# Kernel optimization log

Hardware: AMD Instinct MI355X
Metric: run time of the kernel (lower is better)

Reference implementation:

```python
import jax, jax.numpy as jnp
import numpy as np

N = 4096
DIM = 128      # dim_in
HID = 256      # mlp hidden_dim
K_IN = 8       # k for linear_k

def _knn_edges(dist, k):
    # dist: [n,n]; k nearest neighbors excluding self (matches heapq loop)
    n = dist.shape[0]
    d = jnp.where(jnp.eye(n, dtype=bool), jnp.inf, dist)
    nbr = jax.lax.top_k(-d, k)[1]                     # [n,k] indices of k smallest
    src = jnp.repeat(jnp.arange(n), k)                # res[0] = i
    dst = nbr.reshape(-1)                             # res[1] = neighbor
    return src, dst

def _gcn_conv(x, src, dst, W, b):
    # torch_geometric GCNConv: add self loops + symmetric normalization
    n = x.shape[0]
    loop = jnp.arange(n)
    s = jnp.concatenate([src, loop])
    t = jnp.concatenate([dst, loop])
    xw = x @ W
    deg = jax.ops.segment_sum(jnp.ones(s.shape[0], x.dtype), t, num_segments=n)
    dinv = jax.lax.rsqrt(deg)                         # deg >= 1 due to self loops
    norm = dinv[s] * dinv[t]
    out = jax.ops.segment_sum(norm[:, None] * xw[s], t, num_segments=n)
    return out + b

def _gcn(x, src, dst, Wg1, bg1, Wg2, bg2):
    h = jax.nn.relu(_gcn_conv(x, src, dst, Wg1, bg1))
    h = _gcn_conv(h, src, dst, Wg2, bg2)              # dropout is identity in eval
    return jax.nn.log_softmax(h, axis=1)

def _conv2d(x, w, b):
    y = jax.lax.conv_general_dilated(x, w, (1, 1), 'SAME',
        dimension_numbers=('NCHW', 'OIHW', 'NCHW'))
    return y + b.reshape(1, -1, 1, 1)

def setup_inputs():
    key = jax.random.key(0)
    ks = jax.random.split(key, 20)
    f32 = jnp.float32
    def w(k, shape):
        fan = shape[0]
        return (jax.random.uniform(k, shape, f32) * 2 - 1) * (1.0 / np.sqrt(fan))
    return {
        'data_x_1': jax.random.normal(ks[0], (1, N, 4), f32),
        'data_x_2': jax.random.normal(ks[1], (1, N, K_IN, 4), f32),
        'Wk': w(ks[2], (K_IN, 1)),        'bk': jnp.zeros((1,), f32),
        'Wg1': w(ks[3], (8, DIM // 2)),   'bg1': jnp.zeros((DIM // 2,), f32),
        'Wg2': w(ks[4], (DIM // 2, DIM)), 'bg2': jnp.zeros((DIM,), f32),
        'Wq': w(ks[5], (3 * DIM, DIM)),   'bq': jnp.zeros((DIM,), f32),
        'Wkey': w(ks[6], (3 * DIM, DIM)), 'bkey': jnp.zeros((DIM,), f32),
        'Woff': w(ks[7], (4, DIM)),       'boff': jnp.zeros((DIM,), f32),
        'pw': jnp.full((1,), 0.25, f32),
        'Wf1': w(ks[8], (DIM, HID)),      'bf1': jnp.zeros((HID,), f32),
        'Wf2': w(ks[9], (HID, HID)),      'bf2': jnp.zeros((HID,), f32),
        'Wf3': w(ks[10], (HID, 4)),       'bf3': jnp.zeros((4,), f32),
        'Wcy3': w(ks[11], (1, 1, 1, 3)),  'bcy3': jnp.zeros((1,), f32),
        'Wcx3': w(ks[12], (1, 1, 3, 1)),  'bcx3': jnp.zeros((1,), f32),
        'Wcy5': w(ks[13], (1, 1, 1, 5)),  'bcy5': jnp.zeros((1,), f32),
        'Wcx5': w(ks[14], (1, 1, 5, 1)),  'bcx5': jnp.zeros((1,), f32),
        'Wcy9': w(ks[15], (1, 1, 1, 9)),  'bcy9': jnp.zeros((1,), f32),
        'Wcx9': w(ks[16], (1, 1, 9, 1)),  'bcx9': jnp.zeros((1,), f32),
    }

def reference(data_x_1, data_x_2, Wk, bk, Wg1, bg1, Wg2, bg2, Wq, bq, Wkey, bkey,
              Woff, boff, pw, Wf1, bf1, Wf2, bf2, Wf3, bf3,
              Wcy3, bcy3, Wcx3, bcx3, Wcy5, bcy5, Wcx5, bcx5, Wcy9, bcy9, Wcx9, bcx9):
    # linear_k over k dimension: [1,n,k,4] -> transpose -> [1,n,4,k] -> [1,n,4]
    dx2 = jnp.swapaxes(data_x_2, 2, 3)
    dx2_out = (dx2 @ Wk + bk)[..., 0]
    data_x = jnp.concatenate([data_x_1, dx2_out], axis=2)   # [1,n,8]
    Ot = data_x[:, :, 4:]                                   # [1,n,4]

    pos = data_x[:, :, 0:2]
    diff = pos[:, :, None, :] - pos[:, None, :, :]          # [1,n,n,2]
    distances = jnp.linalg.norm(diff, axis=3)               # [1,n,n]
    maxd = jnp.max(distances, axis=2, keepdims=True)
    oushi_atte = 1.0 - distances / maxd                     # [1,n,n]

    x0 = data_x[0]
    dist0 = jax.lax.stop_gradient(distances[0])             # knn on detached dist
    embs = []
    for kk in (3, 5, 9):
        src, dst = _knn_edges(dist0, kk)
        embs.append(_gcn(x0, src, dst, Wg1, bg1, Wg2, bg2)[None])
    embedding = jnp.concatenate(embs, axis=2)               # [1,n,3*DIM]

    query = embedding @ Wq + bq                             # [1,n,DIM]
    key_t = embedding @ Wkey + bkey
    scores = jnp.einsum('bnd,bmd->bnm', query, key_t) / jnp.sqrt(jnp.float32(DIM))
    A = scores / jnp.max(scores, axis=2, keepdims=True)     # [1,n,n]

    A4 = A[None]                                            # [1,1,n,n]
    c3 = _conv2d(A4, Wcy3, bcy3) + _conv2d(A4, Wcx3, bcx3)
    c5 = _conv2d(A4, Wcy5, bcy5) + _conv2d(A4, Wcx5, bcx5)
    c9 = _conv2d(A4, Wcy9, bcy9) + _conv2d(A4, Wcx9, bcx9)

    A_cat = jnp.concatenate([A, oushi_atte, c3[0], c5[0], c9[0]], axis=2)  # [1,n,5n]
    A_cat = (A_cat - A_cat.min()) / (A_cat.max() - A_cat.min())

    Ot5 = jnp.tile(Ot, (1, 5, 1))                           # [1,5n,4]
    h = jnp.matmul(A_cat, Ot5)                              # [1,n,4]
    h = h @ Woff + boff                                     # [1,n,DIM]
    h = jnp.where(h > 0, h, pw * h)                         # PReLU (scalar weight)
    h = jax.nn.relu(h @ Wf1 + bf1)
    h = jax.nn.relu(h @ Wf2 + bf2)
    return h @ Wf3 + bf3                                    # [1,n,4]
```

## Files before the change

### kernel.cpp

```cpp
#include <hip/hip_runtime.h>
#include <math.h>

#define NN 4096

typedef __bf16 bf16x8 __attribute__((ext_vector_type(8)));
typedef float  f32x4  __attribute__((ext_vector_type(4)));

static __device__ __forceinline__ unsigned enc_f(float f){
    unsigned u = __float_as_uint(f);
    return (u & 0x80000000u) ? ~u : (u | 0x80000000u);
}
static __device__ __forceinline__ float dec_f(unsigned u){
    unsigned b = (u & 0x80000000u) ? (u & 0x7fffffffu) : ~u;
    return __uint_as_float(b);
}
static __device__ __forceinline__ float4 shfl4(float4 v, int src){
    float4 r;
    r.x = __shfl(v.x, src, 64);
    r.y = __shfl(v.y, src, 64);
    r.z = __shfl(v.z, src, 64);
    r.w = __shfl(v.w, src, 64);
    return r;
}
static __device__ __forceinline__ unsigned long long shflx_u64(unsigned long long v, int m){
    unsigned lo = __shfl_xor((unsigned)(v & 0xffffffffu), m, 64);
    unsigned hi = __shfl_xor((unsigned)(v >> 32), m, 64);
    return ((unsigned long long)hi << 32) | lo;
}

__global__ void k_prep(const float* __restrict__ dx1, const float* __restrict__ dx2,
                       const float* __restrict__ Wk, const float* __restrict__ bk,
                       float* __restrict__ x0, float* __restrict__ colsum,
                       float2* __restrict__ pos, float4* __restrict__ otp){
    int n = blockIdx.x*blockDim.x + threadIdx.x;
    if (n >= NN) return;
    float wk[8];
    #pragma unroll
    for (int j=0;j<8;j++) wk[j] = Wk[j];
    float bkv = bk[0];
    float4 d1 = *(const float4*)&dx1[n*4];
    pos[n] = make_float2(d1.x, d1.y);
    #pragma unroll
    for (int c=0;c<4;c++) x0[n*8+c] = (&d1.x)[c];
    float4 ot;
    #pragma unroll
    for (int c=0;c<4;c++){
        float acc = bkv;
        #pragma unroll
        for (int j=0;j<8;j++) acc += dx2[(n*8+j)*4+c]*wk[j];
        x0[n*8+4+c] = acc;
        (&ot.x)[c] = acc;
        atomicAdd(&colsum[c], acc);
    }
    otp[n] = ot;
}

__global__ void k_ty(const float* __restrict__ x0,
        const float* __restrict__ Wcy3, const float* __restrict__ Wcy5, const float* __restrict__ Wcy9,
        float* __restrict__ Ty){
    int j = blockIdx.x*256 + threadIdx.x;
    if (j >= NN) return;
    float Cy[9];
    #pragma unroll
    for (int o=-4;o<=4;o++){
        float c = Wcy9[o+4];
        if (o>=-2 && o<=2) c += Wcy5[o+2];
        if (o>=-1 && o<=1) c += Wcy3[o+1];
        Cy[o+4] = c;
    }
    float4 acc = {0,0,0,0};
    #pragma unroll
    for (int o=-4;o<=4;o++){
        int jj = j - o;
        if ((unsigned)jj < NN){
            float4 ot = *(const float4*)&x0[jj*8+4];
            float c = Cy[o+4];
            acc.x += c*ot.x; acc.y += c*ot.y; acc.z += c*ot.z; acc.w += c*ot.w;
        }
    }
    *(float4*)&Ty[j*4] = acc;
}

#define KCAP 192
__global__ __launch_bounds__(256) void k_dist(const float2* __restrict__ pos,
        const float4* __restrict__ otp,
        float* __restrict__ maxd, int* __restrict__ nbr,
        int* __restrict__ cnt3, int* __restrict__ cnt5, int* __restrict__ cnt9,
        float* __restrict__ dOt){
    __shared__ unsigned long long cbuf[4][KCAP];
    int tid = threadIdx.x;
    int w = tid >> 6, lane = tid & 63;
    int i = blockIdx.x*4 + w;
    float2 pi = pos[i];

    float lmax = 0.f, lmin = INFINITY;
    float4 dacc = {0,0,0,0};
    for (int t=0;t<64;t++){
        int j = (t<<6) | lane;
        float2 p = pos[j];
        float dx = pi.x - p.x, dy = pi.y - p.y;
        float d = sqrtf(dx*dx + dy*dy);
        lmax = fmaxf(lmax, d);
        float4 otj = otp[j];
        dacc.x += d*otj.x; dacc.y += d*otj.y; dacc.z += d*otj.z; dacc.w += d*otj.w;
        if (j != i) lmin = fminf(lmin, d);
    }
    #pragma unroll
    for (int m=1;m<64;m<<=1){
        lmax = fmaxf(lmax, __shfl_xor(lmax, m, 64));
        dacc.x += __shfl_xor(dacc.x, m, 64);
        dacc.y += __shfl_xor(dacc.y, m, 64);
        dacc.z += __shfl_xor(dacc.z, m, 64);
        dacc.w += __shfl_xor(dacc.w, m, 64);
    }
    if (lane==0){
        maxd[i] = lmax;
        *(float4*)&dOt[i*4] = dacc;
    }
    float v = lmin, T = 0.f;
    #pragma unroll
    for (int r=0;r<9;r++){
        float m = v;
        #pragma unroll
        for (int s=1;s<64;s<<=1) m = fminf(m, __shfl_xor(m, s, 64));
        T = m;
        if (v == m) v = INFINITY;
    }

    int base = 0;
    for (int t=0;t<64;t++){
        int j = (t<<6) | lane;
        float2 p = pos[j];
        float dx = pi.x - p.x, dy = pi.y - p.y;
        float d = sqrtf(dx*dx + dy*dy);
        bool pass = (j != i) && (d <= T);
        unsigned long long b = __ballot(pass);
        if (b){
            int pre = __popcll(b & ((1ull<<lane)-1ull));
            int idx = base + pre;
            if (pass && idx < KCAP)
                cbuf[w][idx] = ((unsigned long long)__float_as_uint(d) << 32) | (unsigned)j;
            base += __popcll(b);
        }
    }
    int M = base < KCAP ? base : KCAP;

    unsigned long long c0 = (lane      < M) ? cbuf[w][lane]      : ~0ULL;
    unsigned long long c1 = (lane+64   < M) ? cbuf[w][lane+64]   : ~0ULL;
    unsigned long long c2 = (lane+128  < M) ? cbuf[w][lane+128]  : ~0ULL;
    for (int r=0;r<9;r++){
        unsigned long long mv = c0 < c1 ? c0 : c1;
        mv = mv < c2 ? mv : c2;
        #pragma unroll
        for (int s=1;s<64;s<<=1){
            unsigned long long o = shflx_u64(mv, s);
            if (o < mv) mv = o;
        }
        if (c0 == mv) c0 = ~0ULL;
        else if (c1 == mv) c1 = ~0ULL;
        else if (c2 == mv) c2 = ~0ULL;
        if (lane == 0){
            int j = (int)(mv & 0xffffffffu);
            nbr[i*9+r] = j;
            atomicAdd(&cnt9[j], 1);
            if (r<5) atomicAdd(&cnt5[j], 1);
            if (r<3) atomicAdd(&cnt3[j], 1);
        }
    }
}

__global__ __launch_bounds__(256) void k_scan(const int* __restrict__ cnt3,
        const int* __restrict__ cnt5, const int* __restrict__ cnt9,
        int* __restrict__ offc, float* __restrict__ dinvc){
    __shared__ int part[256];
    int tid = threadIdx.x;
    for (int g=0; g<3; g++){
        const int* cp = g==0?cnt3:(g==1?cnt5:cnt9);
        int base = tid*16;
        int loc[16]; int s=0;
        #pragma unroll
        for (int q=0;q<16;q++){ loc[q]=s; s += cp[base+q]; }
        part[tid]=s; __syncthreads();
        for (int d=1; d<256; d<<=1){
            int v = (tid>=d) ? part[tid-d] : 0;
            __syncthreads();
            part[tid] += v;
            __syncthreads();
        }
        int pre = (tid==0) ? 0 : part[tid-1];
        #pragma unroll
        for (int q=0;q<16;q++){
            offc[g*NN + base + q]  = pre + loc[q];
            dinvc[g*NN + base + q] = rsqrtf((float)cp[base+q] + 1.f);
        }
        __syncthreads();
    }
}

__global__ void k_fill(const int* __restrict__ nbr, const int* __restrict__ offc,
        int* __restrict__ cur, int* __restrict__ rev){
    int i = blockIdx.x*256 + threadIdx.x;
    if (i >= NN) return;
    #pragma unroll
    for (int t=0;t<9;t++){
        int j = nbr[i*9+t];
        int gmin = t<3 ? 0 : (t<5 ? 1 : 2);
        for (int g=gmin; g<3; g++){
            int pos = atomicAdd(&cur[g*NN+j], 1);
            int rb = (g==0) ? 0 : (g==1 ? NN*3 : NN*8);
            rev[rb + offc[g*NN+j] + pos] = i;
        }
    }
}

__global__ void k_y1(const float* __restrict__ x0, const float* __restrict__ Wg1,
                     float* __restrict__ xw){
    int idx = blockIdx.x*256 + threadIdx.x;
    if (idx >= NN*64) return;
    int n = idx>>6, c = idx&63;
    float acc = 0.f;
    #pragma unroll
    for (int k=0;k<8;k++) acc += x0[n*8+k]*Wg1[k*64+c];
    xw[idx] = acc;
}

__global__ __launch_bounds__(256) void k_h1y2(const float* __restrict__ xw,
        const int* __restrict__ offc,
        const int* __restrict__ cnt3, const int* __restrict__ cnt5, const int* __restrict__ cnt9,
        const int* __restrict__ rev, const float* __restrict__ dinvc,
        const float* __restrict__ bg1, const float* __restrict__ Wg2,
        float* __restrict__ y2){
    __shared__ float h1s[12][64];
    int n0 = blockIdx.x*4, tid = threadIdx.x;
    for (int s=tid; s<768; s+=256){
        int p = s>>6, k = s&63, g = p>>2, n = n0+(p&3);
        const int* cp = g==0?cnt3:(g==1?cnt5:cnt9);
        int rb = (g==0) ? 0 : (g==1 ? NN*3 : NN*8);
        int cnt = cp[n];
        int o = rb + offc[g*NN+n];
        float dv = dinvc[g*NN+n];
        float srow = dv*xw[n*64+k];
        for (int e=0;e<cnt;e++){
            int i = rev[o+e];
            srow += dinvc[g*NN+i]*xw[i*64+k];
        }
        float v = dv*srow + bg1[k];
        h1s[p][k] = v>0.f ? v : 0.f;
    }
    __syncthreads();
    int c = tid & 127, ph = tid>>7;
    float a6[6] = {0,0,0,0,0,0};
    for (int k=0;k<64;k++){
        float w = Wg2[k*128+c];
        #pragma unroll
        for (int q=0;q<6;q++) a6[q] += h1s[q*2+ph][k]*w;
    }
    #pragma unroll
    for (int q=0;q<6;q++){
        int p = q*2+ph, g = p>>2, n = n0+(p&3);
        float dv = dinvc[g*NN+n];
        y2[(size_t)g*NN*128 + (size_t)n*128 + c] = dv*a6[q];
    }
}

__global__ __launch_bounds__(128) void k_fin(const float* __restrict__ y2,
        const int* __restrict__ offc,
        const int* __restrict__ cnt3, const int* __restrict__ cnt5, const int* __restrict__ cnt9,
        const int* __restrict__ rev, const float* __restrict__ dinvc,
        const float* __restrict__ bg2, float* __restrict__ emb){
    __shared__ float sm[2], ss[2];
    int b = blockIdx.x;
    int n = b & (NN-1), g = b >> 12;
    const int* cp = g==0?cnt3:(g==1?cnt5:cnt9);
    int rb = (g==0) ? 0 : (g==1 ? NN*3 : NN*8);
    int cnt = cp[n];
    int o = rb + offc[g*NN+n];
    float dv = dinvc[g*NN+n];
    int c = threadIdx.x;
    const float* yg = y2 + (size_t)g*NN*128;
    float s = yg[(size_t)n*128 + c];
    for (int e=0;e<cnt;e++){
        int i = rev[o+e];
        s += yg[(size_t)i*128 + c];
    }
    float v = dv*s + bg2[c];
    float m = v;
    #pragma unroll
    for (int st=1;st<64;st<<=1) m = fmaxf(m, __shfl_xor(m, st, 64));
    if ((c&63)==0) sm[c>>6] = m;
    __syncthreads();
    m = fmaxf(sm[0], sm[1]);
    float e = expf(v - m);
    float t = e;
    #pragma unroll
    for (int st=1;st<64;st<<=1) t += __shfl_xor(t, st, 64);
    if ((c&63)==0) ss[c>>6] = t;
    __syncthreads();
    t = ss[0]+ss[1];
    emb[n*384 + g*128 + c] = v - m - logf(t);
}

__global__ __launch_bounds__(256) void k_qk(const float* __restrict__ emb,
        const float* __restrict__ Wq, const float* __restrict__ bq,
        const float* __restrict__ Wkey, const float* __restrict__ bkey,
        __bf16* __restrict__ qh, __bf16* __restrict__ ql,
        __bf16* __restrict__ kh, __bf16* __restrict__ kl){
    __shared__ float es[8][384];
    int n0 = blockIdx.x*8;
    int tid = threadIdx.x;
    for (int idx=tid; idx<8*384; idx+=256){
        int m = idx/384, k = idx%384;
        es[m][k] = emb[(n0+m)*384+k];
    }
    __syncthreads();
    int c = tid & 127;
    int sel = tid >> 7;
    const float* W = sel ? Wkey : Wq;
    float b = sel ? bkey[c] : bq[c];
    float acc[8];
    #pragma unroll
    for (int m=0;m<8;m++) acc[m]=b;
    for (int k=0;k<384;k++){
        float w = W[k*128+c];
        #pragma unroll
        for (int m=0;m<8;m++) acc[m] += es[m][k]*w;
    }
    __bf16* oh = sel ? kh : qh;
    __bf16* ol = sel ? kl : ql;
    #pragma unroll
    for (int m=0;m<8;m++){
        float v = acc[m];
        __bf16 h = (__bf16)v;
        oh[(size_t)(n0+m)*128+c] = h;
        ol[(size_t)(n0+m)*128+c] = (__bf16)(v - (float)h);
    }
}

__global__ __launch_bounds__(256) void k_scores(
        const __bf16* __restrict__ qh, const __bf16* __restrict__ ql,
        const __bf16* __restrict__ kh, const __bf16* __restrict__ kl,
        float* __restrict__ scores,
        unsigned* __restrict__ rowmaxenc, unsigned* __restrict__ rowminenc){
    int bx = blockIdx.x & 31;
    int by = blockIdx.x >> 5;
    int tid = threadIdx.x;
    int w = tid >> 6, lane = tid & 63;
    int li = lane & 15, g = lane >> 4;
    int r0 = by*128 + (w>>1)*64;
    int c0 = bx*128 + (w&1)*64;

    f32x4 acc[4][4] = {};
    for (int ks=0; ks<4; ++ks){
        int kofs = ks*32 + g*8;
        bf16x8 ah[4], al[4], bh[4], bl[4];
        #pragma unroll
        for (int f=0; f<4; ++f){
            ah[f] = *(const bf16x8*)&qh[(size_t)(r0+f*16+li)*128 + kofs];
            al[f] = *(const bf16x8*)&ql[(size_t)(r0+f*16+li)*128 + kofs];
            bh[f] = *(const bf16x8*)&kh[(size_t)(c0+f*16+li)*128 + kofs];
            bl[f] = *(const bf16x8*)&kl[(size_t)(c0+f*16+li)*128 + kofs];
        }
        #pragma unroll
        for (int fr=0; fr<4; ++fr){
            #pragma unroll
            for (int fc=0; fc<4; ++fc){
                acc[fr][fc] = __builtin_amdgcn_mfma_f32_16x16x32_bf16(ah[fr], bh[fc], acc[fr][fc], 0, 0, 0);
                acc[fr][fc] = __builtin_amdgcn_mfma_f32_16x16x32_bf16(ah[fr], bl[fc], acc[fr][fc], 0, 0, 0);
                acc[fr][fc] = __builtin_amdgcn_mfma_f32_16x16x32_bf16(al[fr], bh[fc], acc[fr][fc], 0, 0, 0);
            }
        }
    }
    #pragma unroll
    for (int fr=0; fr<4; ++fr){
        #pragma unroll
        for (int r=0; r<4; ++r){
            int row = r0 + fr*16 + g*4 + r;
            float mx = -INFINITY, mn = INFINITY;
            #pragma unroll
            for (int fc=0; fc<4; ++fc){
                float v = acc[fr][fc][r];
                scores[(size_t)row*NN + c0 + fc*16 + li] = v;
                mx = fmaxf(mx, v);
                mn = fminf(mn, v);
            }
            #pragma unroll
            for (int s=1; s<16; s<<=1){
                mx = fmaxf(mx, __shfl_xor(mx, s, 64));
                mn = fminf(mn, __shfl_xor(mn, s, 64));
            }
            if (li == 0){
                atomicMax(&rowmaxenc[row], enc_f(mx));
                atomicMin(&rowminenc[row], enc_f(mn));
            }
        }
    }
}

__global__ void k_invr(const unsigned* __restrict__ rowmaxenc, float* __restrict__ invr){
    int i = blockIdx.x*256 + threadIdx.x;
    if (i >= NN) return;
    invr[i] = 1.f/dec_f(rowmaxenc[i]);
}

__global__ __launch_bounds__(256) void k_cconv(const float* __restrict__ scores,
        const float* __restrict__ invr,
        const float* __restrict__ Wcy3, const float* __restrict__ Wcx3,
        const float* __restrict__ Wcy5, const float* __restrict__ Wcx5,
        const float* __restrict__ Wcy9, const float* __restrict__ Wcx9,
        const float* __restrict__ bcy3, const float* __restrict__ bcx3,
        const float* __restrict__ bcy5, const float* __restrict__ bcx5,
        const float* __restrict__ bcy9, const float* __restrict__ bcx9,
        float* __restrict__ mnmx){
    __shared__ float smn[4], smx[4];
    int tid = threadIdx.x;
    int w = tid >> 6, lane = tid & 63;
    int strip = blockIdx.x;
    int i0 = (blockIdx.y*4 + w)*19;
    int colbase = strip*248 - 4 + lane*4;
    bool lv = (colbase >= 0) && (colbase + 3 < NN);
    bool outLane = (lane >= 1) && (lane < 63) && lv;

    float wy3[3],wx3[3],wy5[5],wx5[5],wy9[9],wx9[9];
    #pragma unroll
    for (int t=0;t<3;t++){ wy3[t]=Wcy3[t]; wx3[t]=Wcx3[t]; }
    #pragma unroll
    for (int t=0;t<5;t++){ wy5[t]=Wcy5[t]; wx5[t]=Wcx5[t]; }
    #pragma unroll
    for (int t=0;t<9;t++){ wy9[t]=Wcy9[t]; wx9[t]=Wcx9[t]; }
    float bc3 = bcy3[0]+bcx3[0];
    float bc5 = bcy5[0]+bcx5[0];
    float bc9 = bcy9[0]+bcx9[0];

    float4 win[9];
    float mn = INFINITY, mx = -INFINITY;
    const int laneL = lane - 1, laneR = lane + 1;

    for (int tb = 0; tb < 3; ++tb){
        #pragma unroll
        for (int u = 0; u < 9; ++u){
            int t  = tb*9 + u;
            int ri = i0 - 4 + t;
            float4 a = make_float4(0,0,0,0);
            if (((unsigned)ri < NN) && lv){
                float iv = invr[ri];
                float4 v = *(const float4*)&scores[(size_t)ri*NN + colbase];
                a.x = v.x*iv; a.y = v.y*iv; a.z = v.z*iv; a.w = v.w*iv;
            }
            win[u] = a;
            int ro = i0 + t - 8;
            if (t >= 8 && ro < NN){
                float4 ctr = win[(u+5)%9];
                float4 wl = shfl4(ctr, laneL);
                float4 wr = shfl4(ctr, laneR);
                if (outLane){
                    float cw[12] = {wl.x,wl.y,wl.z,wl.w, ctr.x,ctr.y,ctr.z,ctr.w, wr.x,wr.y,wr.z,wr.w};
                    #pragma unroll
                    for (int c=0;c<4;c++){
                        float cx9 = ((win[(u+1)%9][c]*wx9[0] + win[(u+2)%9][c]*wx9[1]) + (win[(u+3)%9][c]*wx9[2] + win[(u+4)%9][c]*wx9[3]))
                                  + ((win[(u+5)%9][c]*wx9[4] + win[(u+6)%9][c]*wx9[5]) + (win[(u+7)%9][c]*wx9[6] + win[(u+8)%9][c]*wx9[7]))
                                  + win[u][c]*wx9[8];
                        float cx5 = ((win[(u+3)%9][c]*wx5[0] + win[(u+4)%9][c]*wx5[1]) + (win[(u+5)%9][c]*wx5[2] + win[(u+6)%9][c]*wx5[3]))
                                  + win[(u+7)%9][c]*wx5[4];
                        float cx3 = (win[(u+4)%9][c]*wx3[0] + win[(u+5)%9][c]*wx3[1]) + win[(u+6)%9][c]*wx3[2];
                        float cy9 = ((cw[c+0]*wy9[0] + cw[c+1]*wy9[1]) + (cw[c+2]*wy9[2] + cw[c+3]*wy9[3]))
                                  + ((cw[c+4]*wy9[4] + cw[c+5]*wy9[5]) + (cw[c+6]*wy9[6] + cw[c+7]*wy9[7]))
                                  + cw[c+8]*wy9[8];
                        float cy5 = ((cw[c+2]*wy5[0] + cw[c+3]*wy5[1]) + (cw[c+4]*wy5[2] + cw[c+5]*wy5[3]))
                                  + cw[c+6]*wy5[4];
                        float cy3 = (cw[c+3]*wy3[0] + cw[c+4]*wy3[1]) + cw[c+5]*wy3[2];
                        float c3v = cy3+cx3+bc3, c5v = cy5+cx5+bc5, c9v = cy9+cx9+bc9;
                        mn = fminf(mn, fminf(fminf(c3v,c5v),c9v));
                        mx = fmaxf(mx, fmaxf(fmaxf(c3v,c5v),c9v));
                    }
                }
            }
        }
    }
    #pragma unroll
    for (int m=1; m<64; m<<=1){
        mn = fminf(mn, __shfl_xor(mn, m, 64));
        mx = fmaxf(mx, __shfl_xor(mx, m, 64));
    }
    if (lane == 0){ smn[w] = mn; smx[w] = mx; }
    __syncthreads();
    if (tid == 0){
        float a0 = fminf(fminf(smn[0],smn[1]), fminf(smn[2],smn[3]));
        float b0 = fmaxf(fmaxf(smx[0],smx[1]), fmaxf(smx[2],smx[3]));
        int bid = blockIdx.y*gridDim.x + blockIdx.x;
        mnmx[bid] = a0;
        mnmx[1024 + bid] = b0;
    }
}

__global__ __launch_bounds__(256) void k_kot(const __bf16* __restrict__ kh, const __bf16* __restrict__ kl,
        const float* __restrict__ x0, const float* __restrict__ Ty,
        float* __restrict__ kOt){
    __shared__ float red[256][8];
    int d = blockIdx.x, tid = threadIdx.x;
    float a[8] = {0,0,0,0,0,0,0,0};
    for (int j = tid; j < NN; j += 256){
        float kv = (float)kh[(size_t)j*128 + d] + (float)kl[(size_t)j*128 + d];
        float4 ot = *(const float4*)&x0[j*8+4];
        float4 ty = *(const float4*)&Ty[j*4];
        a[0] += kv*ot.x; a[1] += kv*ot.y; a[2] += kv*ot.z; a[3] += kv*ot.w;
        a[4] += kv*ty.x; a[5] += kv*ty.y; a[6] += kv*ty.z; a[7] += kv*ty.w;
    }
    #pragma unroll
    for (int q=0;q<8;q++) red[tid][q] = a[q];
    __syncthreads();
    for (int s=128; s>0; s>>=1){
        if (tid < s){
            #pragma unroll
            for (int q=0;q<8;q++) red[tid][q] += red[tid+s][q];
        }
        __syncthreads();
    }
    if (tid < 8) kOt[d*8 + tid] = red[0][tid];
}

__global__ __launch_bounds__(256) void k_asd(
        const __bf16* __restrict__ qh, const __bf16* __restrict__ ql,
        const float* __restrict__ kOt,
        const unsigned* __restrict__ rowmaxenc, const float* __restrict__ maxd,
        const float* __restrict__ dOt, const float* __restrict__ colsum,
        const float* __restrict__ bcy3, const float* __restrict__ bcx3,
        const float* __restrict__ bcy5, const float* __restrict__ bcx5,
        const float* __restrict__ bcy9, const float* __restrict__ bcx9,
        float* __restrict__ ASdot, float* __restrict__ Bv){
    __shared__ float kst[128*8];
    int tid = threadIdx.x;
    for (int s = tid; s < 1024; s += 256) kst[s] = kOt[s];
    __syncthreads();
    int lane = tid & 63, r = tid >> 6;
    int i = blockIdx.x*4 + r;
    float a[8] = {0,0,0,0,0,0,0,0};
    #pragma unroll
    for (int dd=0; dd<2; ++dd){
        int d = lane + dd*64;
        float qv = (float)qh[(size_t)i*128 + d] + (float)ql[(size_t)i*128 + d];
        #pragma unroll
        for (int q=0;q<8;q++) a[q] += qv * kst[d*8+q];
    }
    #pragma unroll
    for (int m=1; m<64; m<<=1){
        #pragma unroll
        for (int q=0;q<8;q++) a[q] += __shfl_xor(a[q], m, 64);
    }
    if (lane == 0){
        float iv = 1.f/dec_f(rowmaxenc[i]);
        float imv = 1.f/maxd[i];
        float bcsum = bcy3[0]+bcx3[0]+bcy5[0]+bcx5[0]+bcy9[0]+bcx9[0];
        float k = 1.f + bcsum;
        float4 cs = *(const float4*)colsum;
        float4 dv = *(const float4*)&dOt[i*4];
        float4 pa = {iv*a[0], iv*a[1], iv*a[2], iv*a[3]};
        float4 b;
        b.x = cs.x*k - imv*dv.x + iv*a[4];
        b.y = cs.y*k - imv*dv.y + iv*a[5];
        b.z = cs.z*k - imv*dv.z + iv*a[6];
        b.w = cs.w*k - imv*dv.w + iv*a[7];
        *(float4*)&ASdot[i*4] = pa;
        *(float4*)&Bv[i*4]    = b;
    }
}

__global__ __launch_bounds__(256) void k_gmm(const float* __restrict__ mnmx,
        const unsigned* __restrict__ rowminenc, const unsigned* __restrict__ rowmaxenc,
        float* __restrict__ gmm){
    __shared__ float smn[256], smx[256];
    int tid = threadIdx.x;
    float mn = 0.f, mx = 1.f;
    for (int i=tid; i<NN; i+=256){
        float rmx = dec_f(rowmaxenc[i]);
        float q = dec_f(rowminenc[i]) / rmx;
        mn = fminf(mn, fminf(1.f, q));
        mx = fmaxf(mx, fmaxf(1.f, q));
    }
    for (int b=tid; b<918; b+=256){
        mn = fminf(mn, mnmx[b]);
        mx = fmaxf(mx, mnmx[1024+b]);
    }
    smn[tid]=mn; smx[tid]=mx; __syncthreads();
    for (int s=128;s>0;s>>=1){
        if (tid<s){ smn[tid]=fminf(smn[tid],smn[tid+s]); smx[tid]=fmaxf(smx[tid],smx[tid+s]); }
        __syncthreads();
    }
    if (tid==0){ gmm[0]=smn[0]; gmm[1]=smx[0]; }
}

__global__ void k_hfin(const float* __restrict__ ASdot, const float* __restrict__ Bv,
        const float* __restrict__ Wcx3, const float* __restrict__ Wcx5, const float* __restrict__ Wcx9,
        const float* __restrict__ gmm, const float* __restrict__ colsum,
        float* __restrict__ hfin){
    int i = blockIdx.x*256 + threadIdx.x;
    if (i >= NN) return;
    float Cx[9];
    #pragma unroll
    for (int o=-4;o<=4;o++){
        float c = Wcx9[o+4];
        if (o>=-2 && o<=2) c += Wcx5[o+2];
        if (o>=-1 && o<=1) c += Wcx3[o+1];
        Cx[o+4] = c;
    }
    float4 h = *(const float4*)&Bv[i*4];
    float4 a0 = *(const float4*)&ASdot[i*4];
    h.x += a0.x; h.y += a0.y; h.z += a0.z; h.w += a0.w;
    #pragma unroll
    for (int o=-4;o<=4;o++){
        int r = i + o;
        if ((unsigned)r < NN){
            float4 av = *(const float4*)&ASdot[r*4];
            float c = Cx[o+4];
            h.x += c*av.x; h.y += c*av.y; h.z += c*av.z; h.w += c*av.w;
        }
    }
    float mnv = gmm[0], mxv = gmm[1];
    float s = 1.f/(mxv-mnv), oa = -mnv*s;
    float4 cs = *(const float4*)colsum;
    float4 out;
    out.x = s*h.x + 5.f*oa*cs.x;
    out.y = s*h.y + 5.f*oa*cs.y;
    out.z = s*h.z + 5.f*oa*cs.z;
    out.w = s*h.w + 5.f*oa*cs.w;
    *(float4*)&hfin[i*4] = out;
}

__global__ __launch_bounds__(256) void k_mlp(const float* __restrict__ hfin,
        const float* __restrict__ Woff, const float* __restrict__ boff, const float* __restrict__ pw,
        const float* __restrict__ Wf1, const float* __restrict__ bf1,
        const float* __restrict__ Wf2, const float* __restrict__ bf2,
        const float* __restrict__ Wf3, const float* __restrict__ bf3,
        float* __restrict__ out){
    __shared__ float h1[8][128];
    __shared__ float h2[8][256];
    __shared__ float h3[8][256];
    int n0 = blockIdx.x*8, tid = threadIdx.x;
    float p = pw[0];
    {
        int c = tid & 127, mb = (tid>>7)*4;
        #pragma unroll
        for (int mm=0; mm<4; mm++){
            int m = mb+mm;
            float v = boff[c];
            #pragma unroll
            for (int k=0;k<4;k++) v += hfin[(n0+m)*4+k]*Woff[k*128+c];
            h1[m][c] = v>0.f ? v : p*v;
        }
    }
    __syncthreads();
    {
        int c = tid;
        float acc[8];
        #pragma unroll
        for (int m=0;m<8;m++) acc[m] = bf1[c];
        for (int k=0;k<128;k++){
            float w = Wf1[k*256+c];
            #pragma unroll
            for (int m=0;m<8;m++) acc[m] += h1[m][k]*w;
        }
        #pragma unroll
        for (int m=0;m<8;m++) h2[m][c] = acc[m]>0.f?acc[m]:0.f;
    }
    __syncthreads();
    {
        int c = tid;
        float acc[8];
        #pragma unroll
        for (int m=0;m<8;m++) acc[m] = bf2[c];
        for (int k=0;k<256;k++){
            float w = Wf2[k*256+c];
            #pragma unroll
            for (int m=0;m<8;m++) acc[m] += h2[m][k]*w;
        }
        #pragma unroll
        for (int m=0;m<8;m++) h3[m][c] = acc[m]>0.f?acc[m]:0.f;
    }
    __syncthreads();
    int w = tid >> 6, lane = tid & 63;
    #pragma unroll
    for (int mm=0; mm<2; ++mm){
        int m = w*2 + mm;
        float4 acc = {0,0,0,0};
        #pragma unroll
        for (int q=0;q<4;q++){
            int k = lane + q*64;
            float hv = h3[m][k];
            float4 w3 = *(const float4*)&Wf3[k*4];
            acc.x += hv*w3.x; acc.y += hv*w3.y; acc.z += hv*w3.z; acc.w += hv*w3.w;
        }
        #pragma unroll
        for (int s=1; s<64; s<<=1){
            acc.x += __shfl_xor(acc.x, s, 64);
            acc.y += __shfl_xor(acc.y, s, 64);
            acc.z += __shfl_xor(acc.z, s, 64);
            acc.w += __shfl_xor(acc.w, s, 64);
        }
        if (lane == 0){
            float4 o;
            o.x = acc.x + bf3[0]; o.y = acc.y + bf3[1];
            o.z = acc.z + bf3[2]; o.w = acc.w + bf3[3];
            *(float4*)&out[(n0+m)*4] = o;
        }
    }
}

extern "C" void kernel_launch(void* const* d_in, const int* in_sizes, int n_in,
                              void* d_out, int out_size, void* d_ws, size_t ws_size,
                              hipStream_t stream){
    const float* dx1  = (const float*)d_in[0];
    const float* dx2  = (const float*)d_in[1];
    const float* Wk   = (const float*)d_in[2];
    const float* bk   = (const float*)d_in[3];
    const float* Wg1  = (const float*)d_in[4];
    const float* bg1  = (const float*)d_in[5];
    const float* Wg2  = (const float*)d_in[6];
    const float* bg2  = (const float*)d_in[7];
    const float* Wq   = (const float*)d_in[8];
    const float* bq   = (const float*)d_in[9];
    const float* Wkey = (const float*)d_in[10];
    const float* bkey = (const float*)d_in[11];
    const float* Woff = (const float*)d_in[12];
    const float* boff = (const float*)d_in[13];
    const float* pw   = (const float*)d_in[14];
    const float* Wf1  = (const float*)d_in[15];
    const float* bf1  = (const float*)d_in[16];
    const float* Wf2  = (const float*)d_in[17];
    const float* bf2  = (const float*)d_in[18];
    const float* Wf3  = (const float*)d_in[19];
    const float* bf3  = (const float*)d_in[20];
    const float* Wcy3 = (const float*)d_in[21];
    const float* bcy3 = (const float*)d_in[22];
    const float* Wcx3 = (const float*)d_in[23];
    const float* bcx3 = (const float*)d_in[24];
    const float* Wcy5 = (const float*)d_in[25];
    const float* bcy5 = (const float*)d_in[26];
    const float* Wcx5 = (const float*)d_in[27];
    const float* bcx5 = (const float*)d_in[28];
    const float* Wcy9 = (const float*)d_in[29];
    const float* bcy9 = (const float*)d_in[30];
    const float* Wcx9 = (const float*)d_in[31];
    const float* bcx9 = (const float*)d_in[32];

    char* ws = (char*)d_ws;
    size_t off = 0;
    auto alloc = [&](size_t b)->void*{ void* p = ws + off; off += (b + 255) & ~(size_t)255; return p; };

    char* zbase = ws + off;
    float*    colsum    = (float*)   alloc(4*4);
    int*      cnt3      = (int*)     alloc((size_t)NN*4);
    int*      cnt5      = (int*)     alloc((size_t)NN*4);
    int*      cnt9      = (int*)     alloc((size_t)NN*4);
    int*      cur       = (int*)     alloc((size_t)3*NN*4);
    unsigned* rowmaxenc = (unsigned*)alloc((size_t)NN*4);
    size_t zbytes = (size_t)((ws + off) - zbase);
    unsigned* rowminenc = (unsigned*)alloc((size_t)NN*4);

    float*  x0    = (float*) alloc((size_t)NN*8*4);
    float2* pos   = (float2*)alloc((size_t)NN*8);
    float4* otp   = (float4*)alloc((size_t)NN*16);
    float*  maxd  = (float*) alloc((size_t)NN*4);
    int*    nbr   = (int*)   alloc((size_t)NN*9*4);
    int*    offc  = (int*)   alloc((size_t)3*NN*4);
    float*  dinvc = (float*) alloc((size_t)3*NN*4);
    int*    rev   = (int*)   alloc((size_t)NN*17*4);
    float*  xw    = (float*) alloc((size_t)NN*64*4);
    float*  y2    = (float*) alloc((size_t)3*NN*128*4);
    float*  emb   = (float*) alloc((size_t)NN*384*4);
    __bf16* qh    = (__bf16*)alloc((size_t)NN*128*2);
    __bf16* ql    = (__bf16*)alloc((size_t)NN*128*2);
    __bf16* kh    = (__bf16*)alloc((size_t)NN*128*2);
    __bf16* kl    = (__bf16*)alloc((size_t)NN*128*2);
    float* scores = (float*)alloc((size_t)NN*NN*4);
    float* Tyb    = (float*)alloc((size_t)NN*4*4);
    float* invr   = (float*)alloc((size_t)NN*4);
    float* dOt    = (float*)alloc((size_t)NN*4*4);
    float* kOt    = (float*)alloc((size_t)128*8*4);
    float* ASd    = (float*)alloc((size_t)NN*4*4);
    float* Bv     = (float*)alloc((size_t)NN*4*4);
    float* mnmx   = (float*)alloc((size_t)2*1024*4);
    float* gmm    = (float*)alloc(2*4);
    float* hfin   = (float*)alloc((size_t)NN*4*4);
    (void)ws_size; (void)in_sizes; (void)n_in; (void)out_size;

    hipMemsetAsync(zbase, 0, zbytes, stream);
    hipMemsetAsync(rowminenc, 0xFF, (size_t)NN*4, stream);

    k_prep<<<16,256,0,stream>>>(dx1,dx2,Wk,bk,x0,colsum,pos,otp);
    k_ty  <<<16,256,0,stream>>>(x0,Wcy3,Wcy5,Wcy9,Tyb);
    k_dist<<<NN/4,256,0,stream>>>(pos,otp,maxd,nbr,cnt3,cnt5,cnt9,dOt);
    k_scan<<<1,256,0,stream>>>(cnt3,cnt5,cnt9,offc,dinvc);
    k_fill<<<16,256,0,stream>>>(nbr,offc,cur,rev);

    k_y1  <<<NN*64/256,256,0,stream>>>(x0,Wg1,xw);
    k_h1y2<<<NN/4,256,0,stream>>>(xw,offc,cnt3,cnt5,cnt9,rev,dinvc,bg1,Wg2,y2);
    k_fin <<<NN*3,128,0,stream>>>(y2,offc,cnt3,cnt5,cnt9,rev,dinvc,bg2,emb);

    k_qk<<<NN/8,256,0,stream>>>(emb,Wq,bq,Wkey,bkey,qh,ql,kh,kl);
    k_scores<<<1024,256,0,stream>>>(qh,ql,kh,kl,scores,rowmaxenc,rowminenc);
    k_invr<<<16,256,0,stream>>>(rowmaxenc,invr);
    k_kot<<<128,256,0,stream>>>(kh,kl,x0,Tyb,kOt);

    k_cconv<<<dim3(17,54),256,0,stream>>>(scores,invr,
        Wcy3,Wcx3,Wcy5,Wcx5,Wcy9,Wcx9,
        bcy3,bcx3,bcy5,bcx5,bcy9,bcx9, mnmx);
    k_asd<<<NN/4,256,0,stream>>>(qh,ql,kOt,rowmaxenc,maxd,dOt,colsum,
        bcy3,bcx3,bcy5,bcx5,bcy9,bcx9, ASd, Bv);
    k_gmm<<<1,256,0,stream>>>(mnmx,rowminenc,rowmaxenc,gmm);
    k_hfin<<<16,256,0,stream>>>(ASd,Bv,Wcx3,Wcx5,Wcx9,gmm,colsum,hfin);
    k_mlp<<<NN/8,256,0,stream>>>(hfin,Woff,boff,pw,Wf1,bf1,Wf2,bf2,Wf3,bf3,(float*)d_out);
}
```

Measured before the change: 303.5 us.

## Recompute QK scores inside conv kernel instead of materializing full score matrix

The full 4096x4096 fp32 score matrix is no longer written. The first pass now computes only the row max and min. The conv kernel recomputes each 64x64 halo tile of scores with MFMA, scales it by the inverse row max, stages it in LDS and applies the 3/5/9 separable convolutions there to get the min and max. This removes a 64MB write and a 64MB read in exchange for doing the QK matmul twice, with about 30% extra recompute for the halo, plus LDS-based convolution and a larger partial min/max reduction.

```diff
diff --git a/kernel.cpp b/kernel.cpp
--- a/kernel.cpp
+++ b/kernel.cpp
@@ -13,14 +13,6 @@
 static __device__ __forceinline__ float dec_f(unsigned u){
     unsigned b = (u & 0x80000000u) ? (u & 0x7fffffffu) : ~u;
     return __uint_as_float(b);
-}
-static __device__ __forceinline__ float4 shfl4(float4 v, int src){
-    float4 r;
-    r.x = __shfl(v.x, src, 64);
-    r.y = __shfl(v.y, src, 64);
-    r.z = __shfl(v.z, src, 64);
-    r.w = __shfl(v.w, src, 64);
-    return r;
 }
 static __device__ __forceinline__ unsigned long long shflx_u64(unsigned long long v, int m){
     unsigned lo = __shfl_xor((unsigned)(v & 0xffffffffu), m, 64);
@@ -336,34 +328,36 @@
     }
 }
 
-__global__ __launch_bounds__(256) void k_scores(
+__global__ __launch_bounds__(256) void k_qkmm(
         const __bf16* __restrict__ qh, const __bf16* __restrict__ ql,
         const __bf16* __restrict__ kh, const __bf16* __restrict__ kl,
-        float* __restrict__ scores,
         unsigned* __restrict__ rowmaxenc, unsigned* __restrict__ rowminenc){
-    int bx = blockIdx.x & 31;
-    int by = blockIdx.x >> 5;
+    int bx = blockIdx.x & 63;
+    int by = blockIdx.x >> 6;
     int tid = threadIdx.x;
     int w = tid >> 6, lane = tid & 63;
     int li = lane & 15, g = lane >> 4;
     int r0 = by*128 + (w>>1)*64;
-    int c0 = bx*128 + (w&1)*64;
-
-    f32x4 acc[4][4] = {};
+    int c0 = bx*64  + (w&1)*32;
+
+    f32x4 acc[4][2] = {};
     for (int ks=0; ks<4; ++ks){
         int kofs = ks*32 + g*8;
-        bf16x8 ah[4], al[4], bh[4], bl[4];
+        bf16x8 ah[4], al[4], bh[2], bl[2];
         #pragma unroll
         for (int f=0; f<4; ++f){
             ah[f] = *(const bf16x8*)&qh[(size_t)(r0+f*16+li)*128 + kofs];
             al[f] = *(const bf16x8*)&ql[(size_t)(r0+f*16+li)*128 + kofs];
+        }
+        #pragma unroll
+        for (int f=0; f<2; ++f){
             bh[f] = *(const bf16x8*)&kh[(size_t)(c0+f*16+li)*128 + kofs];
             bl[f] = *(const bf16x8*)&kl[(size_t)(c0+f*16+li)*128 + kofs];
         }
         #pragma unroll
         for (int fr=0; fr<4; ++fr){
             #pragma unroll
-            for (int fc=0; fc<4; ++fc){
+            for (int fc=0; fc<2; ++fc){
                 acc[fr][fc] = __builtin_amdgcn_mfma_f32_16x16x32_bf16(ah[fr], bh[fc], acc[fr][fc], 0, 0, 0);
                 acc[fr][fc] = __builtin_amdgcn_mfma_f32_16x16x32_bf16(ah[fr], bl[fc], acc[fr][fc], 0, 0, 0);
                 acc[fr][fc] = __builtin_amdgcn_mfma_f32_16x16x32_bf16(al[fr], bh[fc], acc[fr][fc], 0, 0, 0);
@@ -375,14 +369,8 @@
         #pragma unroll
         for (int r=0; r<4; ++r){
             int row = r0 + fr*16 + g*4 + r;
-            float mx = -INFINITY, mn = INFINITY;
-            #pragma unroll
-            for (int fc=0; fc<4; ++fc){
-                float v = acc[fr][fc][r];
-                scores[(size_t)row*NN + c0 + fc*16 + li] = v;
-                mx = fmaxf(mx, v);
-                mn = fminf(mn, v);
-            }
+            float mx = fmaxf(acc[fr][0][r], acc[fr][1][r]);
+            float mn = fminf(acc[fr][0][r], acc[fr][1][r]);
             #pragma unroll
             for (int s=1; s<16; s<<=1){
                 mx = fmaxf(mx, __shfl_xor(mx, s, 64));
@@ -402,7 +390,9 @@
     invr[i] = 1.f/dec_f(rowmaxenc[i]);
 }
 
-__global__ __launch_bounds__(256) void k_cconv(const float* __restrict__ scores,
+__global__ __launch_bounds__(256) void k_convf(
+        const __bf16* __restrict__ qh, const __bf16* __restrict__ ql,
+        const __bf16* __restrict__ kh, const __bf16* __restrict__ kl,
         const float* __restrict__ invr,
         const float* __restrict__ Wcy3, const float* __restrict__ Wcx3,
         const float* __restrict__ Wcy5, const float* __restrict__ Wcx5,
@@ -411,14 +401,55 @@
         const float* __restrict__ bcy5, const float* __restrict__ bcx5,
         const float* __restrict__ bcy9, const float* __restrict__ bcx9,
         float* __restrict__ mnmx){
+    __shared__ float As[64][68];
     __shared__ float smn[4], smx[4];
+    int bx = blockIdx.x, by = blockIdx.y;
+    int i0 = by*56 - 4;
+    int j0 = bx*56 - 4;
     int tid = threadIdx.x;
     int w = tid >> 6, lane = tid & 63;
-    int strip = blockIdx.x;
-    int i0 = (blockIdx.y*4 + w)*19;
-    int colbase = strip*248 - 4 + lane*4;
-    bool lv = (colbase >= 0) && (colbase + 3 < NN);
-    bool outLane = (lane >= 1) && (lane < 63) && lv;
+    int li = lane & 15, g = lane >> 4;
+
+    f32x4 acc[4] = {};
+    {
+        int col = j0 + w*16 + li;
+        int colc = col < 0 ? 0 : (col > NN-1 ? NN-1 : col);
+        for (int ks=0; ks<4; ++ks){
+            int kofs = ks*32 + g*8;
+            bf16x8 ah[4], al[4], bh, bl;
+            #pragma unroll
+            for (int f=0; f<4; ++f){
+                int row = i0 + f*16 + li;
+                int rowc = row < 0 ? 0 : (row > NN-1 ? NN-1 : row);
+                ah[f] = *(const bf16x8*)&qh[(size_t)rowc*128 + kofs];
+                al[f] = *(const bf16x8*)&ql[(size_t)rowc*128 + kofs];
+            }
+            bh = *(const bf16x8*)&kh[(size_t)colc*128 + kofs];
+            bl = *(const bf16x8*)&kl[(size_t)colc*128 + kofs];
+            #pragma unroll
+            for (int fr=0; fr<4; ++fr){
+                acc[fr] = __builtin_amdgcn_mfma_f32_16x16x32_bf16(ah[fr], bh, acc[fr], 0, 0, 0);
+                acc[fr] = __builtin_amdgcn_mfma_f32_16x16x32_bf16(ah[fr], bl, acc[fr], 0, 0, 0);
+                acc[fr] = __builtin_amdgcn_mfma_f32_16x16x32_bf16(al[fr], bh, acc[fr], 0, 0, 0);
+            }
+        }
+    }
+    {
+        int gcol = j0 + w*16 + li;
+        bool cok = (unsigned)gcol < NN;
+        #pragma unroll
+        for (int fr=0; fr<4; ++fr){
+            #pragma unroll
+            for (int r=0; r<4; ++r){
+                int lr = fr*16 + g*4 + r;
+                int grow = i0 + lr;
+                float v = 0.f;
+                if (cok && (unsigned)grow < NN) v = acc[fr][r] * invr[grow];
+                As[lr][w*16 + li] = v;
+            }
+        }
+    }
+    __syncthreads();
 
     float wy3[3],wx3[3],wy5[5],wx5[5],wy9[9],wx9[9];
     #pragma unroll
@@ -431,49 +462,30 @@
     float bc5 = bcy5[0]+bcx5[0];
     float bc9 = bcy9[0]+bcx9[0];
 
-    float4 win[9];
     float mn = INFINITY, mx = -INFINITY;
-    const int laneL = lane - 1, laneR = lane + 1;
-
-    for (int tb = 0; tb < 3; ++tb){
-        #pragma unroll
-        for (int u = 0; u < 9; ++u){
-            int t  = tb*9 + u;
-            int ri = i0 - 4 + t;
-            float4 a = make_float4(0,0,0,0);
-            if (((unsigned)ri < NN) && lv){
-                float iv = invr[ri];
-                float4 v = *(const float4*)&scores[(size_t)ri*NN + colbase];
-                a.x = v.x*iv; a.y = v.y*iv; a.z = v.z*iv; a.w = v.w*iv;
+    for (int idx = tid; idx < 56*56; idx += 256){
+        int r = (idx/56) + 4, c = (idx%56) + 4;
+        int grow = i0 + r, gcol = j0 + c;
+        if (grow < NN && gcol < NN){
+            float cx9=0.f, cx5=0.f, cx3=0.f;
+            #pragma unroll
+            for (int u=0;u<9;++u){
+                float rv = As[r-4+u][c];
+                cx9 += rv*wx9[u];
+                if (u>=2 && u<=6) cx5 += rv*wx5[u-2];
+                if (u>=3 && u<=5) cx3 += rv*wx3[u-3];
             }
-            win[u] = a;
-            int ro = i0 + t - 8;
-            if (t >= 8 && ro < NN){
-                float4 ctr = win[(u+5)%9];
-                float4 wl = shfl4(ctr, laneL);
-                float4 wr = shfl4(ctr, laneR);
-                if (outLane){
-                    float cw[12] = {wl.x,wl.y,wl.z,wl.w, ctr.x,ctr.y,ctr.z,ctr.w, wr.x,wr.y,wr.z,wr.w};
-                    #pragma unroll
-                    for (int c=0;c<4;c++){
-                        float cx9 = ((win[(u+1)%9][c]*wx9[0] + win[(u+2)%9][c]*wx9[1]) + (win[(u+3)%9][c]*wx9[2] + win[(u+4)%9][c]*wx9[3]))
-                                  + ((win[(u+5)%9][c]*wx9[4] + win[(u+6)%9][c]*wx9[5]) + (win[(u+7)%9][c]*wx9[6] + win[(u+8)%9][c]*wx9[7]))
-                                  + win[u][c]*wx9[8];
-                        float cx5 = ((win[(u+3)%9][c]*wx5[0] + win[(u+4)%9][c]*wx5[1]) + (win[(u+5)%9][c]*wx5[2] + win[(u+6)%9][c]*wx5[3]))
-                                  + win[(u+7)%9][c]*wx5[4];
-                        float cx3 = (win[(u+4)%9][c]*wx3[0] + win[(u+5)%9][c]*wx3[1]) + win[(u+6)%9][c]*wx3[2];
-                        float cy9 = ((cw[c+0]*wy9[0] + cw[c+1]*wy9[1]) + (cw[c+2]*wy9[2] + cw[c+3]*wy9[3]))
-                                  + ((cw[c+4]*wy9[4] + cw[c+5]*wy9[5]) + (cw[c+6]*wy9[6] + cw[c+7]*wy9[7]))
-                                  + cw[c+8]*wy9[8];
-                        float cy5 = ((cw[c+2]*wy5[0] + cw[c+3]*wy5[1]) + (cw[c+4]*wy5[2] + cw[c+5]*wy5[3]))
-                                  + cw[c+6]*wy5[4];
-                        float cy3 = (cw[c+3]*wy3[0] + cw[c+4]*wy3[1]) + cw[c+5]*wy3[2];
-                        float c3v = cy3+cx3+bc3, c5v = cy5+cx5+bc5, c9v = cy9+cx9+bc9;
-                        mn = fminf(mn, fminf(fminf(c3v,c5v),c9v));
-                        mx = fmaxf(mx, fmaxf(fmaxf(c3v,c5v),c9v));
-                    }
-                }
+            float cy9=0.f, cy5=0.f, cy3=0.f;
+            #pragma unroll
+            for (int u=0;u<9;++u){
+                float cv = As[r][c-4+u];
+                cy9 += cv*wy9[u];
+                if (u>=2 && u<=6) cy5 += cv*wy5[u-2];
+                if (u>=3 && u<=5) cy3 += cv*wy3[u-3];
             }
+            float c3v = cy3+cx3+bc3, c5v = cy5+cx5+bc5, c9v = cy9+cx9+bc9;
+            mn = fminf(mn, fminf(fminf(c3v,c5v),c9v));
+            mx = fmaxf(mx, fmaxf(fmaxf(c3v,c5v),c9v));
         }
     }
     #pragma unroll
@@ -486,9 +498,9 @@
     if (tid == 0){
         float a0 = fminf(fminf(smn[0],smn[1]), fminf(smn[2],smn[3]));
         float b0 = fmaxf(fmaxf(smx[0],smx[1]), fmaxf(smx[2],smx[3]));
-        int bid = blockIdx.y*gridDim.x + blockIdx.x;
+        int bid = by*74 + bx;
         mnmx[bid] = a0;
-        mnmx[1024 + bid] = b0;
+        mnmx[5632 + bid] = b0;
     }
 }
 
@@ -521,7 +533,7 @@
 __global__ __launch_bounds__(256) void k_asd(
         const __bf16* __restrict__ qh, const __bf16* __restrict__ ql,
         const float* __restrict__ kOt,
-        const unsigned* __restrict__ rowmaxenc, const float* __restrict__ maxd,
+        const float* __restrict__ invr, const float* __restrict__ maxd,
         const float* __restrict__ dOt, const float* __restrict__ colsum,
         const float* __restrict__ bcy3, const float* __restrict__ bcx3,
         const float* __restrict__ bcy5, const float* __restrict__ bcx5,
@@ -547,7 +559,7 @@
         for (int q=0;q<8;q++) a[q] += __shfl_xor(a[q], m, 64);
     }
     if (lane == 0){
-        float iv = 1.f/dec_f(rowmaxenc[i]);
+        float iv = invr[i];
         float imv = 1.f/maxd[i];
         float bcsum = bcy3[0]+bcx3[0]+bcy5[0]+bcx5[0]+bcy9[0]+bcx9[0];
         float k = 1.f + bcsum;
@@ -576,9 +588,9 @@
         mn = fminf(mn, fminf(1.f, q));
         mx = fmaxf(mx, fmaxf(1.f, q));
     }
-    for (int b=tid; b<918; b+=256){
+    for (int b=tid; b<5476; b+=256){
         mn = fminf(mn, mnmx[b]);
-        mx = fmaxf(mx, mnmx[1024+b]);
+        mx = fmaxf(mx, mnmx[5632+b]);
     }
     smn[tid]=mn; smx[tid]=mx; __syncthreads();
     for (int s=128;s>0;s>>=1){
@@ -770,14 +782,13 @@
     __bf16* ql    = (__bf16*)alloc((size_t)NN*128*2);
     __bf16* kh    = (__bf16*)alloc((size_t)NN*128*2);
     __bf16* kl    = (__bf16*)alloc((size_t)NN*128*2);
-    float* scores = (float*)alloc((size_t)NN*NN*4);
     float* Tyb    = (float*)alloc((size_t)NN*4*4);
     float* invr   = (float*)alloc((size_t)NN*4);
     float* dOt    = (float*)alloc((size_t)NN*4*4);
     float* kOt    = (float*)alloc((size_t)128*8*4);
     float* ASd    = (float*)alloc((size_t)NN*4*4);
     float* Bv     = (float*)alloc((size_t)NN*4*4);
-    float* mnmx   = (float*)alloc((size_t)2*1024*4);
+    float* mnmx   = (float*)alloc((size_t)2*5632*4);
     float* gmm    = (float*)alloc(2*4);
     float* hfin   = (float*)alloc((size_t)NN*4*4);
     (void)ws_size; (void)in_sizes; (void)n_in; (void)out_size;
@@ -796,14 +807,14 @@
     k_fin <<<NN*3,128,0,stream>>>(y2,offc,cnt3,cnt5,cnt9,rev,dinvc,bg2,emb);
 
     k_qk<<<NN/8,256,0,stream>>>(emb,Wq,bq,Wkey,bkey,qh,ql,kh,kl);
-    k_scores<<<1024,256,0,stream>>>(qh,ql,kh,kl,scores,rowmaxenc,rowminenc);
+    k_qkmm<<<2048,256,0,stream>>>(qh,ql,kh,kl,rowmaxenc,rowminenc);
     k_invr<<<16,256,0,stream>>>(rowmaxenc,invr);
     k_kot<<<128,256,0,stream>>>(kh,kl,x0,Tyb,kOt);
 
-    k_cconv<<<dim3(17,54),256,0,stream>>>(scores,invr,
+    k_convf<<<dim3(74,74),256,0,stream>>>(qh,ql,kh,kl,invr,
         Wcy3,Wcx3,Wcy5,Wcx5,Wcy9,Wcx9,
         bcy3,bcx3,bcy5,bcx5,bcy9,bcx9, mnmx);
-    k_asd<<<NN/4,256,0,stream>>>(qh,ql,kOt,rowmaxenc,maxd,dOt,colsum,
+    k_asd<<<NN/4,256,0,stream>>>(qh,ql,kOt,invr,maxd,dOt,colsum,
         bcy3,bcx3,bcy5,bcx5,bcy9,bcx9, ASd, Bv);
     k_gmm<<<1,256,0,stream>>>(mnmx,rowminenc,rowmaxenc,gmm);
     k_hfin<<<16,256,0,stream>>>(ASd,Bv,Wcx3,Wcx5,Wcx9,gmm,colsum,hfin);
```

New measurement: 400.0 us. +31.8%, slower.
